# Kernel optimization log

Hardware: AMD Instinct MI355X
Metric: run time of the kernel (lower is better)

Reference implementation:

```python
import jax, jax.numpy as jnp
import numpy as np

LN_EPS = 1e-5


def setup_inputs() -> dict:
    key = jax.random.key(0)
    k1, k2, k3, k4 = jax.random.split(key, 4)
    B, S, F, H = 128, 1024, 16, 512
    x = jax.random.normal(k1, (B, S, F), dtype=jnp.float32)
    # stacked per-feature Linear(1,H): W[i] = feature_projs[i].weight[:,0], b[i] = bias
    W = jax.random.normal(k2, (F, H), dtype=jnp.float32) * (1.0 / np.sqrt(F))
    b = jax.random.normal(k3, (F, H), dtype=jnp.float32) * 0.02
    emb = jax.random.normal(k4, (S, H), dtype=jnp.float32)  # num_stabilizers == S
    gamma = jnp.ones((H,), dtype=jnp.float32)
    beta = jnp.zeros((H,), dtype=jnp.float32)
    return {"x": x, "W": W, "b": b, "emb": emb, "gamma": gamma, "beta": beta}


def reference(x, W, b, emb, gamma, beta):
    # sum_i Linear_i(x[...,i:i+1]) == x @ W + sum_i b_i  (single fused GEMM)
    h = jnp.einsum("bsf,fh->bsh", x, W) + b.sum(axis=0)
    # index embedding: idx = arange(S), broadcast over batch
    h = h + emb[: x.shape[1]]  # (B,S,H) + (S,H)
    # LayerNorm over last dim
    mu = h.mean(axis=-1, keepdims=True)
    var = h.var(axis=-1, keepdims=True)
    hn = (h - mu) * jax.lax.rsqrt(var + LN_EPS)
    return hn * gamma + beta
```

## Files before the change

kernel.cpp:

```cpp
#include <hip/hip_runtime.h>

#define LN_EPS 1e-5f

static constexpr int Hc  = 512;
static constexpr int Fc  = 16;
static constexpr int Sc  = 1024;
static constexpr int RPW = 16;

__global__ void bsum_kernel(const float* __restrict__ b, float* __restrict__ bsum) {
    int h = blockIdx.x * 64 + threadIdx.x;
    float s = 0.f;
#pragma unroll
    for (int i = 0; i < Fc; ++i) s += b[i * Hc + h];
    bsum[h] = s;
}

template <int CTRL, int RMASK>
__device__ __forceinline__ float dpp_add(float v) {
    int t = __builtin_amdgcn_update_dpp(0, __float_as_int(v), CTRL, RMASK, 0xf, true);
    return v + __int_as_float(t);
}
__device__ __forceinline__ float wave_sum64(float v) {
    v = dpp_add<0x111, 0xf>(v);
    v = dpp_add<0x112, 0xf>(v);
    v = dpp_add<0x114, 0xf>(v);
    v = dpp_add<0x118, 0xf>(v);
    v = dpp_add<0x142, 0xa>(v);
    v = dpp_add<0x143, 0xc>(v);
    return __int_as_float(__builtin_amdgcn_readlane(__float_as_int(v), 63));
}
__device__ __forceinline__ float rdlane(float v, int l) {
    return __int_as_float(__builtin_amdgcn_readlane(__float_as_int(v), l));
}

__device__ __forceinline__ unsigned rne16(float f) {
    unsigned u = __float_as_uint(f);
    return (u + 0x7fffu + ((u >> 16) & 1u)) >> 16;
}
__device__ __forceinline__ unsigned pack2(float lo, float hi) {
    return rne16(lo) | (rne16(hi) << 16);
}
__device__ __forceinline__ float lo_f(unsigned p) { return __uint_as_float(p << 16); }
__device__ __forceinline__ float hi_f(unsigned p) { return __uint_as_float(p); }

__global__ __launch_bounds__(256) void fused_kernel(
    const float* __restrict__ x, const float* __restrict__ W,
    const float* __restrict__ emb, const float* __restrict__ bsum,
    const float* __restrict__ gamma, const float* __restrict__ beta,
    float* __restrict__ out)
{
    const int lane = threadIdx.x & 63;
    const int wid  = (blockIdx.x << 2) | (threadIdx.x >> 6);
    const int s    = wid & (Sc - 1);
    const int g    = wid >> 10;
    const int h0 = lane * 4, h1 = h0 + 256;

    unsigned p00[Fc], p01[Fc], p10[Fc], p11[Fc];
#pragma unroll
    for (int i = 0; i < Fc; ++i) {
        const float4 wa = *reinterpret_cast<const float4*>(&W[i * Hc + h0]);
        const float4 wb = *reinterpret_cast<const float4*>(&W[i * Hc + h1]);
        p00[i] = pack2(wa.x, wa.y);
        p01[i] = pack2(wa.z, wa.w);
        p10[i] = pack2(wb.x, wb.y);
        p11[i] = pack2(wb.z, wb.w);
    }

    const int sub = lane >> 4, i16 = lane & 15;
    float xq0, xq1, xq2, xq3;
    {
        const size_t xoff = (size_t)s * Fc + i16;
        xq0 = __builtin_nontemporal_load(&x[(size_t)(g * 16 +  0 + sub) * Sc * Fc + xoff]);
        xq1 = __builtin_nontemporal_load(&x[(size_t)(g * 16 +  4 + sub) * Sc * Fc + xoff]);
        xq2 = __builtin_nontemporal_load(&x[(size_t)(g * 16 +  8 + sub) * Sc * Fc + xoff]);
        xq3 = __builtin_nontemporal_load(&x[(size_t)(g * 16 + 12 + sub) * Sc * Fc + xoff]);
    }

    const float4 g0  = *reinterpret_cast<const float4*>(&gamma[h0]);
    const float4 g1  = *reinterpret_cast<const float4*>(&gamma[h1]);
    const float4 be0 = *reinterpret_cast<const float4*>(&beta[h0]);
    const float4 be1 = *reinterpret_cast<const float4*>(&beta[h1]);
    float4 ebs0, ebs1;
    {
        const float4 e0  = *reinterpret_cast<const float4*>(&emb[(size_t)s * Hc + h0]);
        const float4 e1  = *reinterpret_cast<const float4*>(&emb[(size_t)s * Hc + h1]);
        const float4 bs0 = *reinterpret_cast<const float4*>(&bsum[h0]);
        const float4 bs1 = *reinterpret_cast<const float4*>(&bsum[h1]);
        ebs0.x = e0.x + bs0.x; ebs0.y = e0.y + bs0.y; ebs0.z = e0.z + bs0.z; ebs0.w = e0.w + bs0.w;
        ebs1.x = e1.x + bs1.x; ebs1.y = e1.y + bs1.y; ebs1.z = e1.z + bs1.z; ebs1.w = e1.w + bs1.w;
    }

#pragma unroll
    for (int t = 0; t < RPW; ++t) {
        const float xsrc = (t >> 2) == 0 ? xq0 : (t >> 2) == 1 ? xq1 : (t >> 2) == 2 ? xq2 : xq3;

        float4 a0 = ebs0, a1 = ebs1;
#pragma unroll
        for (int i = 0; i < Fc; ++i) {
            const float xi = rdlane(xsrc, (t & 3) * 16 + i);
            a0.x = fmaf(xi, lo_f(p00[i]), a0.x);
            a0.y = fmaf(xi, hi_f(p00[i]), a0.y);
            a0.z = fmaf(xi, lo_f(p01[i]), a0.z);
            a0.w = fmaf(xi, hi_f(p01[i]), a0.w);
            a1.x = fmaf(xi, lo_f(p10[i]), a1.x);
            a1.y = fmaf(xi, hi_f(p10[i]), a1.y);
            a1.z = fmaf(xi, lo_f(p11[i]), a1.z);
            a1.w = fmaf(xi, hi_f(p11[i]), a1.w);
        }

        float psum = a0.x + a0.y + a0.z + a0.w + a1.x + a1.y + a1.z + a1.w;
        float pssq = fmaf(a0.x, a0.x, fmaf(a0.y, a0.y, fmaf(a0.z, a0.z, a0.w * a0.w)));
        pssq = fmaf(a1.x, a1.x, fmaf(a1.y, a1.y, fmaf(a1.z, a1.z, fmaf(a1.w, a1.w, pssq))));

        const float sum = wave_sum64(psum);
        const float ssq = wave_sum64(pssq);

        const float mean = sum * (1.0f / 512.0f);
        const float var  = ssq * (1.0f / 512.0f) - mean * mean;
        const float rs   = rsqrtf(var + LN_EPS);
        const float nmrs = -mean * rs;

        float4 r0, r1;
        r0.x = fmaf(fmaf(a0.x, rs, nmrs), g0.x, be0.x);
        r0.y = fmaf(fmaf(a0.y, rs, nmrs), g0.y, be0.y);
        r0.z = fmaf(fmaf(a0.z, rs, nmrs), g0.z, be0.z);
        r0.w = fmaf(fmaf(a0.w, rs, nmrs), g0.w, be0.w);
        r1.x = fmaf(fmaf(a1.x, rs, nmrs), g1.x, be1.x);
        r1.y = fmaf(fmaf(a1.y, rs, nmrs), g1.y, be1.y);
        r1.z = fmaf(fmaf(a1.z, rs, nmrs), g1.z, be1.z);
        r1.w = fmaf(fmaf(a1.w, rs, nmrs), g1.w, be1.w);

        float* orow = out + ((size_t)(g * 16 + t) * Sc + s) * Hc;
        *reinterpret_cast<float4*>(&orow[h0]) = r0;
        *reinterpret_cast<float4*>(&orow[h1]) = r1;
    }
}

extern "C" void kernel_launch(void* const* d_in, const int* in_sizes, int n_in,
                              void* d_out, int out_size, void* d_ws, size_t ws_size,
                              hipStream_t stream) {
    const float* x     = (const float*)d_in[0];
    const float* W     = (const float*)d_in[1];
    const float* b     = (const float*)d_in[2];
    const float* emb   = (const float*)d_in[3];
    const float* gamma = (const float*)d_in[4];
    const float* beta  = (const float*)d_in[5];
    float* out  = (float*)d_out;
    float* bsum = (float*)d_ws;

    bsum_kernel<<<Hc / 64, 64, 0, stream>>>(b, bsum);

    const int blocks = (8 * Sc) / 4;
    fused_kernel<<<blocks, 256, 0, stream>>>(x, W, emb, bsum, gamma, beta, out);
}
```

Measured before the change: 66.05 us.

## Use packed fp16 dot2 for feature projection and pair adjacent x features

Packs W as fp16 pairs along the feature dimension and packs neighbouring x features into half2 using a DPP row shift. The inner loop then runs v_dot2 instructions with fp32 accumulation, halving both the FMA count and the readlane count per row. It also adds a minimum-blocks hint to launch_bounds. The risk is lower precision, since x is also rounded to fp16 and both conversions truncate toward zero; the kernel was likely store-bound, which would limit any gain.

```diff
diff --git a/kernel.cpp b/kernel.cpp
--- a/kernel.cpp
+++ b/kernel.cpp
@@ -1,6 +1,8 @@
 #include <hip/hip_runtime.h>
 
 #define LN_EPS 1e-5f
+
+typedef __fp16 h2 __attribute__((ext_vector_type(2)));
 
 static constexpr int Hc  = 512;
 static constexpr int Fc  = 16;
@@ -29,21 +31,23 @@
     v = dpp_add<0x143, 0xc>(v);
     return __int_as_float(__builtin_amdgcn_readlane(__float_as_int(v), 63));
 }
-__device__ __forceinline__ float rdlane(float v, int l) {
-    return __int_as_float(__builtin_amdgcn_readlane(__float_as_int(v), l));
+__device__ __forceinline__ int rdlane_i(int v, int l) {
+    return __builtin_amdgcn_readlane(v, l);
 }
 
-__device__ __forceinline__ unsigned rne16(float f) {
-    unsigned u = __float_as_uint(f);
-    return (u + 0x7fffu + ((u >> 16) & 1u)) >> 16;
+__device__ __forceinline__ float fdot2(h2 a, h2 b, float c) {
+#if __has_builtin(__builtin_amdgcn_fdot2)
+    return __builtin_amdgcn_fdot2(a, b, c, false);
+#else
+    return fmaf((float)a.x, (float)b.x, fmaf((float)a.y, (float)b.y, c));
+#endif
 }
-__device__ __forceinline__ unsigned pack2(float lo, float hi) {
-    return rne16(lo) | (rne16(hi) << 16);
+
+__device__ __forceinline__ h2 pkrtz(float lo, float hi) {
+    return __builtin_amdgcn_cvt_pkrtz(lo, hi);
 }
-__device__ __forceinline__ float lo_f(unsigned p) { return __uint_as_float(p << 16); }
-__device__ __forceinline__ float hi_f(unsigned p) { return __uint_as_float(p); }
 
-__global__ __launch_bounds__(256) void fused_kernel(
+__global__ __launch_bounds__(256, 2) void fused_kernel(
     const float* __restrict__ x, const float* __restrict__ W,
     const float* __restrict__ emb, const float* __restrict__ bsum,
     const float* __restrict__ gamma, const float* __restrict__ beta,
@@ -55,25 +59,39 @@
     const int g    = wid >> 10;
     const int h0 = lane * 4, h1 = h0 + 256;
 
-    unsigned p00[Fc], p01[Fc], p10[Fc], p11[Fc];
+    h2 wp[8][8];
 #pragma unroll
-    for (int i = 0; i < Fc; ++i) {
-        const float4 wa = *reinterpret_cast<const float4*>(&W[i * Hc + h0]);
-        const float4 wb = *reinterpret_cast<const float4*>(&W[i * Hc + h1]);
-        p00[i] = pack2(wa.x, wa.y);
-        p01[i] = pack2(wa.z, wa.w);
-        p10[i] = pack2(wb.x, wb.y);
-        p11[i] = pack2(wb.z, wb.w);
+    for (int j = 0; j < 8; ++j) {
+        const float4 a0 = *reinterpret_cast<const float4*>(&W[(2 * j    ) * Hc + h0]);
+        const float4 a1 = *reinterpret_cast<const float4*>(&W[(2 * j + 1) * Hc + h0]);
+        const float4 b0 = *reinterpret_cast<const float4*>(&W[(2 * j    ) * Hc + h1]);
+        const float4 b1 = *reinterpret_cast<const float4*>(&W[(2 * j + 1) * Hc + h1]);
+        wp[j][0] = pkrtz(a0.x, a1.x);
+        wp[j][1] = pkrtz(a0.y, a1.y);
+        wp[j][2] = pkrtz(a0.z, a1.z);
+        wp[j][3] = pkrtz(a0.w, a1.w);
+        wp[j][4] = pkrtz(b0.x, b1.x);
+        wp[j][5] = pkrtz(b0.y, b1.y);
+        wp[j][6] = pkrtz(b0.z, b1.z);
+        wp[j][7] = pkrtz(b0.w, b1.w);
     }
 
     const int sub = lane >> 4, i16 = lane & 15;
-    float xq0, xq1, xq2, xq3;
+    int xp0, xp1, xp2, xp3;
     {
         const size_t xoff = (size_t)s * Fc + i16;
-        xq0 = __builtin_nontemporal_load(&x[(size_t)(g * 16 +  0 + sub) * Sc * Fc + xoff]);
-        xq1 = __builtin_nontemporal_load(&x[(size_t)(g * 16 +  4 + sub) * Sc * Fc + xoff]);
-        xq2 = __builtin_nontemporal_load(&x[(size_t)(g * 16 +  8 + sub) * Sc * Fc + xoff]);
-        xq3 = __builtin_nontemporal_load(&x[(size_t)(g * 16 + 12 + sub) * Sc * Fc + xoff]);
+        float q0 = __builtin_nontemporal_load(&x[(size_t)(g * 16 +  0 + sub) * Sc * Fc + xoff]);
+        float q1 = __builtin_nontemporal_load(&x[(size_t)(g * 16 +  4 + sub) * Sc * Fc + xoff]);
+        float q2 = __builtin_nontemporal_load(&x[(size_t)(g * 16 +  8 + sub) * Sc * Fc + xoff]);
+        float q3 = __builtin_nontemporal_load(&x[(size_t)(g * 16 + 12 + sub) * Sc * Fc + xoff]);
+        auto nb = [](float v) {
+            return __int_as_float(__builtin_amdgcn_update_dpp(
+                0, __float_as_int(v), 0x101, 0xf, 0xf, true));
+        };
+        xp0 = __builtin_bit_cast(int, pkrtz(q0, nb(q0)));
+        xp1 = __builtin_bit_cast(int, pkrtz(q1, nb(q1)));
+        xp2 = __builtin_bit_cast(int, pkrtz(q2, nb(q2)));
+        xp3 = __builtin_bit_cast(int, pkrtz(q3, nb(q3)));
     }
 
     const float4 g0  = *reinterpret_cast<const float4*>(&gamma[h0]);
@@ -92,20 +110,20 @@
 
 #pragma unroll
     for (int t = 0; t < RPW; ++t) {
-        const float xsrc = (t >> 2) == 0 ? xq0 : (t >> 2) == 1 ? xq1 : (t >> 2) == 2 ? xq2 : xq3;
+        const int xsrc = (t >> 2) == 0 ? xp0 : (t >> 2) == 1 ? xp1 : (t >> 2) == 2 ? xp2 : xp3;
 
         float4 a0 = ebs0, a1 = ebs1;
 #pragma unroll
-        for (int i = 0; i < Fc; ++i) {
-            const float xi = rdlane(xsrc, (t & 3) * 16 + i);
-            a0.x = fmaf(xi, lo_f(p00[i]), a0.x);
-            a0.y = fmaf(xi, hi_f(p00[i]), a0.y);
-            a0.z = fmaf(xi, lo_f(p01[i]), a0.z);
-            a0.w = fmaf(xi, hi_f(p01[i]), a0.w);
-            a1.x = fmaf(xi, lo_f(p10[i]), a1.x);
-            a1.y = fmaf(xi, hi_f(p10[i]), a1.y);
-            a1.z = fmaf(xi, lo_f(p11[i]), a1.z);
-            a1.w = fmaf(xi, hi_f(p11[i]), a1.w);
+        for (int j = 0; j < 8; ++j) {
+            const h2 xj = __builtin_bit_cast(h2, rdlane_i(xsrc, (t & 3) * 16 + 2 * j));
+            a0.x = fdot2(xj, wp[j][0], a0.x);
+            a0.y = fdot2(xj, wp[j][1], a0.y);
+            a0.z = fdot2(xj, wp[j][2], a0.z);
+            a0.w = fdot2(xj, wp[j][3], a0.w);
+            a1.x = fdot2(xj, wp[j][4], a1.x);
+            a1.y = fdot2(xj, wp[j][5], a1.y);
+            a1.z = fdot2(xj, wp[j][6], a1.z);
+            a1.w = fdot2(xj, wp[j][7], a1.w);
         }
 
         float psum = a0.x + a0.y + a0.z + a0.w + a1.x + a1.y + a1.z + a1.w;
```

Measured after the change: 68.12 us. +3.1%, slower.
